# Optimization experiments

Hardware: AMD Instinct MI355X
Metric: run time of the kernel (lower is better)

The kernel has to match this reference:

```python
import jax, jax.numpy as jnp
import numpy as np

B, N, H, L, K = 8, 2048, 256, 4, 16
G, M0, M1, C = 512, 256, 128, 128
EPS = 1e-5


def _rn(k, shape, scale):
    return jax.random.normal(k, shape, jnp.float32) * jnp.float32(scale)


def setup_inputs() -> dict:
    key = jax.random.key(0)
    ks = jax.random.split(key, 16)
    z, o = jnp.zeros, jnp.ones
    return {
        "x": jax.random.normal(ks[0], (B, N, 3), jnp.float32),
        "batch": jnp.repeat(jnp.arange(B, dtype=jnp.int32)[:, None], N, axis=1),
        "Wf": _rn(ks[1], (3, H), 0.5), "bf": z(H),
        "Wnn": _rn(ks[2], (H, H), H ** -0.5), "bnn": z(H),
        "g1": o((L, H)), "b1": z((L, H)),
        "We": _rn(ks[3], (L, 2 * H, H), (2 * H) ** -0.5), "be": z((L, H)),
        "g2": o((L, H)), "b2": z((L, H)),
        "Wl": _rn(ks[4], (L, H, H), H ** -0.5), "bl": z((L, H)),
        "alpha": _rn(ks[5], (L,), 0.1),
        "gg": o(H), "bgb": z(H),
        "Wg": _rn(ks[6], (H, G), H ** -0.5), "bg2": z(G),
        "Wm1": _rn(ks[7], (G, M0), G ** -0.5), "bm1": z(M0),
        "Wm2": _rn(ks[8], (M0, M1), M0 ** -0.5), "bm2": z(M1),
        "Wm3": _rn(ks[9], (M1, C), M1 ** -0.5), "bm3": z(C),
    }


def _bn(x, g, b):
    # BatchNorm1d training-mode math over all nodes (axes B,N), per channel
    m = x.mean(axis=(0, 1))
    v = x.var(axis=(0, 1))
    return (x - m) * jax.lax.rsqrt(v + EPS) * g + b


def _dgcnn(x, We, be):
    # dynamic kNN graph in feature space, per cloud; x: [B,N,H]
    sq = jnp.sum(x * x, axis=-1)                                  # [B,N]
    d = sq[:, :, None] + sq[:, None, :] - 2.0 * jnp.einsum('bnd,bmd->bnm', x, x)
    idx = jax.lax.top_k(-d, K)[1]                                 # [B,N,K] (includes self)
    x_j = jax.vmap(lambda xb, ib: xb[ib])(x, idx)                 # [B,N,K,H]
    x_i = x[:, :, None, :]
    e = jnp.concatenate([jnp.broadcast_to(x_i, x_j.shape), x_j - x_i], axis=-1)
    msg = jnp.einsum('bnkf,fh->bnkh', e, We) + be                 # edge MLP
    return jnp.max(msg, axis=2)                                   # max aggregate


def _forward(x, Wf, bf, Wnn, bnn, g1, b1, We, be, g2, b2, Wl, bl, alpha,
             gg, bgb, Wg, bg2, Wm1, bm1, Wm2, bm2, Wm3, bm3):
    h = x @ Wf + bf                                               # ffm_x (Linear, scale=None)
    for i in range(L):
        t = h @ Wnn + bnn if i == 0 else h                        # nn_x only on first layer
        t = jax.nn.relu(_bn(t, g1[i], b1[i]))
        t = _dgcnn(t, We[i], be[i])
        t = jax.nn.relu(_bn(t, g2[i], b2[i]))
        t = t @ Wl[i] + bl[i]
        h = h + alpha[i] * t                                      # ResidualCoefficient
    t = jax.nn.relu(_bn(h, gg, bgb)) @ Wg + bg2
    p = jnp.max(t, axis=1)                                        # global max pool -> [B,G]
    p = jax.nn.relu(p @ Wm1 + bm1)
    p = jax.nn.relu(p @ Wm2 + bm2)
    return p @ Wm3 + bm3                                          # [B, n_components]


def reference(x, batch, Wf, bf, Wnn, bnn, g1, b1, We, be, g2, b2, Wl, bl, alpha,
              gg, bgb, Wg, bg2, Wm1, bm1, Wm2, bm2, Wm3, bm3):
    # batch ids are implied by the dense [B,N] layout; kept for signature fidelity
    del batch
    return _forward(x, Wf, bf, Wnn, bnn, g1, b1, We, be, g2, b2, Wl, bl, alpha,
                    gg, bgb, Wg, bg2, Wm1, bm1, Wm2, bm2, Wm3, bm3)
```

## Files before the change

### kernel.cpp

```cpp
#include <hip/hip_runtime.h>
#include <cfloat>

#define B_  8
#define N_  2048
#define H_  256
#define L_  4
#define K_  16
#define G_  512
#define M0_ 256
#define M1_ 128
#define C_  128
#define BN_ 16384
#define KP_ 768

typedef unsigned short ushort_t;
typedef __attribute__((ext_vector_type(8))) short short8;
typedef __attribute__((ext_vector_type(4))) float f32x4;

#define OFF_H     ((size_t)0)
#define OFF_APACK ((size_t)16777216)
#define OFF_WPK   ((size_t)46137344)
#define OFF_BCA   ((size_t)52035584)
#define OFF_STA   ((size_t)52043776)
#define OFF_SQ    ((size_t)67108864)
#define OFF_IDX   ((size_t)67174400)
#define OFF_P0    ((size_t)68231168)
#define OFF_D     ((size_t)69206016)
#define OFF_T     (OFF_D + (size_t)0)
#define OFF_UV    (OFF_D + (size_t)50331648)
#define OFF_PMAX  (OFF_D + (size_t)84672512)
#define WS_NEEDED ((size_t)203423744)

#define WPK_WNN   0
#define WPK_WL    256
#define WPK_WG    1280
#define WPK_QCAT  1792

static __device__ __forceinline__ ushort_t f2bf(float f) {
    unsigned u = __float_as_uint(f);
    unsigned r = (u + 0x7fffu + ((u >> 16) & 1u)) >> 16;
    return (ushort_t)r;
}
static __device__ __forceinline__ float bf2f(ushort_t h) {
    return __uint_as_float(((unsigned)h) << 16);
}
static __device__ __forceinline__ void pack3(float v, ushort_t* A, size_t base, int f) {
    ushort_t hi = f2bf(v);
    ushort_t lo = f2bf(v - bf2f(hi));
    A[base + f] = hi; A[base + H_ + f] = lo; A[base + 2 * H_ + f] = hi;
}


__global__ void feat_pack(const float* __restrict__ x, const float* __restrict__ Wf,
                          const float* __restrict__ bfv, float* __restrict__ h,
                          ushort_t* __restrict__ Ap) {
    int pt = blockIdx.x;
    int f  = threadIdx.x;
    float x0 = x[pt * 3 + 0], x1 = x[pt * 3 + 1], x2 = x[pt * 3 + 2];
    float v = x0 * Wf[f] + x1 * Wf[H_ + f] + x2 * Wf[2 * H_ + f] + bfv[f];
    h[(size_t)pt * H_ + f] = v;
    pack3(v, Ap, (size_t)pt * KP_, f);
}

__global__ void pack_all(const float* __restrict__ Wnn, const float* __restrict__ Wl,
                         const float* __restrict__ Wg, const float* __restrict__ We,
                         const float* __restrict__ be, ushort_t* __restrict__ Qp,
                         float* __restrict__ bcat) {
    int row = blockIdx.x, k = threadIdx.x;
    float w;
    if (row < 1792) {
        const float* W; int Nd, n;
        if (row < 256)        { W = Wnn; Nd = 256; n = row; }
        else if (row < 1280)  { int l = (row - 256) >> 8;
                                W = Wl + (size_t)l * (H_ * H_); Nd = 256; n = (row - 256) & 255; }
        else                  { W = Wg; Nd = 512; n = row - 1280; }
        w = W[(size_t)k * Nd + n];
    } else {
        int rr = row - 1792; int l = rr >> 9; int n = rr & 511;
        const float* We_l = We + (size_t)l * 2 * H_ * H_;
        if (n < H_) w = We_l[(size_t)k * H_ + n] - We_l[(size_t)H_ * H_ + (size_t)k * H_ + n];
        else        w = We_l[(size_t)H_ * H_ + (size_t)k * H_ + (n - H_)];
        if (k == 0) bcat[l * 512 + n] = (n < H_) ? be[l * H_ + n] : 0.f;
    }
    ushort_t hi = f2bf(w), lo = f2bf(w - bf2f(hi));
    size_t base = (size_t)row * KP_;
    Qp[base + k] = hi; Qp[base + H_ + k] = hi; Qp[base + 2 * H_ + k] = lo;
}

__global__ __launch_bounds__(256) void mfma_gemm(
    const ushort_t* __restrict__ P, const ushort_t* __restrict__ Q,
    const float* __restrict__ aux, float* __restrict__ out,
    int Kd, int ldOut, int mode, const float* __restrict__ resid,
    const float* __restrict__ alphap, int aidx, double* __restrict__ stats,
    int nx) {
    __shared__ __align__(16) ushort_t As[128 * 32];
    __shared__ __align__(16) ushort_t Bs[128 * 32];
    __shared__ float cs1[4][64], cs2[4][64];
    int i0, j0;
    if (nx) {
        int blk = blockIdx.x;
        int z = blk & 7;
        int rest = blk >> 3;
        int xb = rest % nx;
        int ys = rest / nx;
        i0 = (z * 16 + ys) * 128;
        j0 = xb * 128;
    } else {
        i0 = blockIdx.y * 128; j0 = blockIdx.x * 128;
    }
    int tid = threadIdx.x;
    int lane = tid & 63, wave = tid >> 6;
    int wm = wave & 1, wn = wave >> 1;
    int m16 = lane & 15, kq = (lane >> 4) * 8;

    f32x4 acc[4][4];
    f32x4 zero = {0.f, 0.f, 0.f, 0.f};
#pragma unroll
    for (int i = 0; i < 4; ++i)
#pragma unroll
        for (int j = 0; j < 4; ++j) acc[i][j] = zero;

    int srow = tid >> 2;
    int skc  = (tid & 3) * 8;

    for (int k0 = 0; k0 < Kd; k0 += 32) {
#pragma unroll
        for (int s = 0; s < 2; ++s) {
            int row = srow + s * 64;
            const ushort_t* gpA = P + (size_t)(i0 + row) * Kd + k0 + skc;
            const ushort_t* gpB = Q + (size_t)(j0 + row) * Kd + k0 + skc;
            __builtin_amdgcn_global_load_lds(
                (const __attribute__((address_space(1))) void*)gpA,
                (__attribute__((address_space(3))) void*)(As + (size_t)(wave * 64 + s * 256) * 8),
                16, 0, 0);
            __builtin_amdgcn_global_load_lds(
                (const __attribute__((address_space(1))) void*)gpB,
                (__attribute__((address_space(3))) void*)(Bs + (size_t)(wave * 64 + s * 256) * 8),
                16, 0, 0);
        }
        __syncthreads();
        short8 af[4], bfr[4];
#pragma unroll
        for (int fi = 0; fi < 4; ++fi)
            af[fi] = *(const short8*)(As + (wm * 64 + fi * 16 + m16) * 32 + kq);
#pragma unroll
        for (int fj = 0; fj < 4; ++fj)
            bfr[fj] = *(const short8*)(Bs + (wn * 64 + fj * 16 + m16) * 32 + kq);
#pragma unroll
        for (int fi = 0; fi < 4; ++fi)
#pragma unroll
            for (int fj = 0; fj < 4; ++fj)
                acc[fi][fj] = __builtin_amdgcn_mfma_f32_16x16x32_bf16(
                    af[fi], bfr[fj], acc[fi][fj], 0, 0, 0);
        __syncthreads();
    }
    float alpha = (mode == 2) ? alphap[aidx] : 0.f;
    int rbase = i0 + wm * 64 + (lane >> 4) * 4;
    int cbase = j0 + wn * 64 + m16;
    float s1[4] = {0.f, 0.f, 0.f, 0.f}, s2[4] = {0.f, 0.f, 0.f, 0.f};
#pragma unroll
    for (int fi = 0; fi < 4; ++fi) {
#pragma unroll
        for (int fj = 0; fj < 4; ++fj) {
            int c = cbase + fj * 16;
            float a = aux[c];
#pragma unroll
            for (int r = 0; r < 4; ++r) {
                int gr = rbase + fi * 16 + r;
                size_t oidx = (size_t)gr * ldOut + c;
                float val;
                if (mode == 2) val = resid[oidx] + alpha * (acc[fi][fj][r] + a);
                else           val = acc[fi][fj][r] + a;
                out[oidx] = val;
                s1[fj] += val; s2[fj] += val * val;
            }
        }
    }
    if (stats) {
#pragma unroll
        for (int fj = 0; fj < 4; ++fj) {
            float a1 = s1[fj], a2 = s2[fj];
            a1 += __shfl_xor(a1, 16); a1 += __shfl_xor(a1, 32);
            a2 += __shfl_xor(a2, 16); a2 += __shfl_xor(a2, 32);
            if ((lane >> 4) == 0) {
                cs1[wave][fj * 16 + m16] = a1;
                cs2[wave][fj * 16 + m16] = a2;
            }
        }
        __syncthreads();
        if (tid < 128) {
            int wnl = tid >> 6, cl = tid & 63;
            float t1 = cs1[2 * wnl][cl] + cs1[2 * wnl + 1][cl];
            float t2 = cs2[2 * wnl][cl] + cs2[2 * wnl + 1][cl];
            int c = j0 + tid;
            atomicAdd(&stats[c], (double)t1);
            atomicAdd(&stats[H_ + c], (double)t2);
        }
    }
}

__global__ __launch_bounds__(256) void gram_sym(const ushort_t* __restrict__ Ap,
                                                const float* __restrict__ sqb,
                                                float* __restrict__ D) {
    __shared__ __align__(16) ushort_t As[128 * 32];
    __shared__ __align__(16) ushort_t Bs[128 * 32];
    __shared__ __align__(16) float stg[4][1280];
    int blk = blockIdx.x;
    int z = blk & 7;
    int p = blk >> 3;
    int bi = 0, rem = p;
    while (rem >= 16 - bi) { rem -= 16 - bi; ++bi; }
    int bj = bi + rem;
    const ushort_t* Pz = Ap + (size_t)z * N_ * KP_;
    const float* sqz = sqb + (size_t)z * N_;
    float* Dz = D + (size_t)z * N_ * N_;
    int i0 = bi * 128, j0 = bj * 128;

    int tid = threadIdx.x;
    int lane = tid & 63, wave = tid >> 6;
    int wm = wave & 1, wn = wave >> 1;
    int m16 = lane & 15, q4 = lane >> 4;
    int kq = q4 * 8;

    f32x4 acc[4][4];
    f32x4 zero = {0.f, 0.f, 0.f, 0.f};
#pragma unroll
    for (int i = 0; i < 4; ++i)
#pragma unroll
        for (int j = 0; j < 4; ++j) acc[i][j] = zero;

    int srow = tid >> 2;
    int skc  = (tid & 3) * 8;

    for (int k0 = 0; k0 < KP_; k0 += 32) {
        int kb = (k0 < 256) ? k0 : ((k0 < 512) ? k0 + 256 : k0 - 256);
#pragma unroll
        for (int s = 0; s < 2; ++s) {
            int row = srow + s * 64;
            const ushort_t* gpA = Pz + (size_t)(i0 + row) * KP_ + k0 + skc;
            const ushort_t* gpB = Pz + (size_t)(j0 + row) * KP_ + kb + skc;
            __builtin_amdgcn_global_load_lds(
                (const __attribute__((address_space(1))) void*)gpA,
                (__attribute__((address_space(3))) void*)(As + (size_t)(wave * 64 + s * 256) * 8),
                16, 0, 0);
            __builtin_amdgcn_global_load_lds(
                (const __attribute__((address_space(1))) void*)gpB,
                (__attribute__((address_space(3))) void*)(Bs + (size_t)(wave * 64 + s * 256) * 8),
                16, 0, 0);
        }
        __syncthreads();
        short8 af[4], bfr[4];
#pragma unroll
        for (int fi = 0; fi < 4; ++fi)
            af[fi] = *(const short8*)(As + (wm * 64 + fi * 16 + m16) * 32 + kq);
#pragma unroll
        for (int fj = 0; fj < 4; ++fj)
            bfr[fj] = *(const short8*)(Bs + (wn * 64 + fj * 16 + m16) * 32 + kq);
#pragma unroll
        for (int fi = 0; fi < 4; ++fi)
#pragma unroll
            for (int fj = 0; fj < 4; ++fj)
                acc[fi][fj] = __builtin_amdgcn_mfma_f32_16x16x32_bf16(
                    af[fi], bfr[fj], acc[fi][fj], 0, 0, 0);
        __syncthreads();
    }

    float* sg = stg[wave];
    float scl[4];
#pragma unroll
    for (int fj = 0; fj < 4; ++fj) scl[fj] = sqz[j0 + wn * 64 + fj * 16 + m16];
    float sr[4][4];
#pragma unroll
    for (int fi = 0; fi < 4; ++fi) {
        float4 s4 = *(const float4*)(sqz + i0 + wm * 64 + fi * 16 + q4 * 4);
        sr[fi][0] = s4.x; sr[fi][1] = s4.y; sr[fi][2] = s4.z; sr[fi][3] = s4.w;
    }

    int rr = lane >> 2, cc = lane & 3;
#pragma unroll
    for (int fi = 0; fi < 4; ++fi) {
#pragma unroll
        for (int fj = 0; fj < 4; ++fj)
#pragma unroll
            for (int r = 0; r < 4; ++r)
                sg[(q4 * 4 + r) * 68 + fj * 16 + m16] = scl[fj] - 2.f * acc[fi][fj][r];
        float* drow = Dz + (size_t)(i0 + wm * 64 + fi * 16 + rr) * N_ + j0 + wn * 64;
#pragma unroll
        for (int t = 0; t < 4; ++t) {
            int chunk = cc + 4 * t;
            f32x4 o = *(const f32x4*)(sg + rr * 68 + chunk * 4);
            __builtin_nontemporal_store(o, (f32x4*)(drow + chunk * 4));
        }
    }

    if (bi != bj) {
#pragma unroll
        for (int fi = 0; fi < 4; ++fi) {
#pragma unroll
            for (int fj = 0; fj < 4; ++fj)
#pragma unroll
                for (int r = 0; r < 4; ++r)
                    sg[(fj * 16 + m16) * 20 + q4 * 4 + r] =
                        sr[fi][r] - 2.f * acc[fi][fj][r];
            int chunk = lane & 3;
#pragma unroll
            for (int u = 0; u < 4; ++u) {
                int cr = (lane >> 2) + 16 * u;
                f32x4 o = *(const f32x4*)(sg + cr * 20 + chunk * 4);
                __builtin_nontemporal_store(o,
                    (f32x4*)(Dz + (size_t)(j0 + wn * 64 + cr) * N_ +
                             i0 + wm * 64 + fi * 16 + chunk * 4));
            }
        }
    }
}

__global__ __launch_bounds__(256) void topk16(const float* __restrict__ D,
                                              int* __restrict__ idxb) {
    __shared__ unsigned long long cand[4][256];
    __shared__ int cnt[4];
    int w = threadIdx.x >> 6, lane = threadIdx.x & 63;
    int row = blockIdx.x * 4 + w;
    const float* dp = D + (size_t)row * N_;
    unsigned sk[32];
#pragma unroll
    for (int t = 0; t < 8; ++t) {
        f32x4 v4 = __builtin_nontemporal_load((const f32x4*)(dp + t * 256 + lane * 4));
#pragma unroll
        for (int j = 0; j < 4; ++j) {
            unsigned u = __float_as_uint(v4[j]);
            sk[t * 4 + j] = (u & 0x80000000u) ? ~u : (u | 0x80000000u);
        }
    }
    if (lane == 0) cnt[w] = 0;
    unsigned vm = sk[0];
#pragma unroll
    for (int i = 1; i < 32; ++i) vm = min(vm, sk[i]);
#pragma unroll
    for (int k = 2; k <= 64; k <<= 1) {
#pragma unroll
        for (int j = k >> 1; j > 0; j >>= 1) {
            unsigned pv = __shfl_xor(vm, j);
            bool up = ((lane & k) == 0);
            bool lower = ((lane & j) == 0);
            unsigned mn = min(vm, pv), mx = max(vm, pv);
            vm = (lower == up) ? mn : mx;
        }
    }
    unsigned T = __shfl(vm, 15);
    __syncthreads();
#pragma unroll
    for (int i = 0; i < 32; ++i) {
        if (sk[i] <= T) {
            unsigned col = (unsigned)((i >> 2) * 256 + lane * 4 + (i & 3));
            int s = atomicAdd(&cnt[w], 1);
            if (s < 256) cand[w][s] = ((unsigned long long)sk[i] << 32) | col;
        }
    }
    __syncthreads();
    int cn = cnt[w];
    if (cn <= 64) {
        unsigned long long mykey = (lane < cn) ? cand[w][lane] : ~0ull;
        for (int it = 0; it < 16; ++it) {
            unsigned long long best = mykey;
#pragma unroll
            for (int off = 32; off; off >>= 1) {
                unsigned long long o = __shfl_xor(best, off);
                if (o < best) best = o;
            }
            if (mykey == best) mykey = ~0ull;
            if (lane == 0) idxb[row * 16 + it] = (int)(unsigned)(best & 0xffffffffu);
        }
    } else if (cn <= 256) {
        for (int it = 0; it < 16; ++it) {
            unsigned long long best = ~0ull;
            for (int i = lane; i < cn; i += 64) {
                unsigned long long c = cand[w][i];
                if (c < best) best = c;
            }
#pragma unroll
            for (int off = 32; off; off >>= 1) {
                unsigned long long o = __shfl_xor(best, off);
                if (o < best) best = o;
            }
            for (int i = lane; i < cn; i += 64)
                if (cand[w][i] == best) cand[w][i] = ~0ull;
            if (lane == 0) idxb[row * 16 + it] = (int)(unsigned)(best & 0xffffffffu);
        }
    } else {
        unsigned mask = 0;
        for (int it = 0; it < 16; ++it) {
            unsigned long long key = ~0ull;
#pragma unroll
            for (int i = 0; i < 32; ++i) {
                if (!((mask >> i) & 1u)) {
                    unsigned long long k2 = ((unsigned long long)sk[i] << 32) |
                        (unsigned)((i >> 2) * 256 + lane * 4 + (i & 3));
                    if (k2 < key) key = k2;
                }
            }
#pragma unroll
            for (int off = 32; off; off >>= 1) {
                unsigned long long o = __shfl_xor(key, off);
                if (o < key) key = o;
            }
            unsigned jc = (unsigned)(key & 0xffffffffu);
            int li = ((jc & 255) >> 2);
            int ii = ((jc >> 8) << 2) | (jc & 3);
            if (lane == li) mask |= 1u << ii;
            if (lane == 0) idxb[row * 16 + it] = (int)jc;
        }
    }
}

__global__ void gather_max(const float* __restrict__ uv, const int* __restrict__ idxb,
                           float* __restrict__ outp, double* __restrict__ stats) {
    int blk = blockIdx.x;
    int b = blk & 7;
    int strip = blk >> 3;
    int r0 = b * N_ + strip * 32;
    int f = threadIdx.x;
    float s1 = 0.f, s2 = 0.f;
    for (int rr = 0; rr < 32; ++rr) {
        int row = r0 + rr;
        const int* ip = idxb + row * 16;
        float m = -FLT_MAX;
#pragma unroll
        for (int k = 0; k < 16; ++k) {
            int j = ip[k];
            m = fmaxf(m, uv[((size_t)((b << 11) + j)) * 512 + 256 + f]);
        }
        float v = uv[(size_t)row * 512 + f] + m;
        outp[(size_t)row * H_ + f] = v;
        s1 += v; s2 += v * v;
    }
    atomicAdd(&stats[f], (double)s1);
    atomicAdd(&stats[H_ + f], (double)s2);
}

__global__ void bn_zero(double* s) { s[(size_t)blockIdx.x * 512 + threadIdx.x] = 0.0; }

__global__ void bn_apply_pack(const float* __restrict__ X, const double* __restrict__ sums,
                              const float* __restrict__ g, const float* __restrict__ b,
                              ushort_t* __restrict__ Ap, float* __restrict__ sq) {
    __shared__ float scsh[512];
    int tid = threadIdx.x;
    {
        double m  = sums[tid] / (double)BN_;
        double var = sums[H_ + tid] / (double)BN_ - m * m;
        double inv = 1.0 / sqrt(var + 1e-5);
        float sc = g[tid] * (float)inv;
        scsh[tid] = sc;
        scsh[H_ + tid] = b[tid] - (float)m * sc;
    }
    __syncthreads();
    int row = blockIdx.x * 8 + (tid >> 5);
    int f0  = (tid & 31) * 8;
    const float* xp = X + (size_t)row * H_ + f0;
    f32x4 x0 = *(const f32x4*)(xp);
    f32x4 x1 = *(const f32x4*)(xp + 4);
    f32x4 sc0 = *(const f32x4*)(scsh + f0);
    f32x4 sc1 = *(const f32x4*)(scsh + f0 + 4);
    f32x4 sh0 = *(const f32x4*)(scsh + H_ + f0);
    f32x4 sh1 = *(const f32x4*)(scsh + H_ + f0 + 4);
    float v[8];
#pragma unroll
    for (int i = 0; i < 4; ++i) {
        v[i]     = fmaxf(x0[i] * sc0[i] + sh0[i], 0.f);
        v[i + 4] = fmaxf(x1[i] * sc1[i] + sh1[i], 0.f);
    }
    short8 hi8, lo8;
#pragma unroll
    for (int i = 0; i < 8; ++i) {
        ushort_t hi = f2bf(v[i]);
        ushort_t lo = f2bf(v[i] - bf2f(hi));
        hi8[i] = (short)hi; lo8[i] = (short)lo;
    }
    ushort_t* ap = Ap + (size_t)row * KP_ + f0;
    *(short8*)(ap)            = hi8;
    *(short8*)(ap + H_)       = lo8;
    *(short8*)(ap + 2 * H_)   = hi8;
    if (sq) {
        float s = 0.f;
#pragma unroll
        for (int i = 0; i < 8; ++i) s += v[i] * v[i];
#pragma unroll
        for (int off = 16; off; off >>= 1) s += __shfl_down(s, off, 32);
        if ((tid & 31) == 0) sq[row] = s;
    }
}

__global__ void maxpool1(const float* __restrict__ y, float* __restrict__ pmax) {
    int b = blockIdx.x, gc = blockIdx.y, nc = blockIdx.z;
    int g = gc * 256 + threadIdx.x;
    const float* yb = y + ((size_t)b * N_ + (size_t)nc * 128) * G_;
    float m = -FLT_MAX;
    for (int n = 0; n < 128; ++n) m = fmaxf(m, yb[(size_t)n * G_ + g]);
    pmax[((size_t)(b * 16 + nc)) * G_ + g] = m;
}

__global__ void maxpool2(const float* __restrict__ pmax, float* __restrict__ p) {
    int b = blockIdx.x;
    int g = blockIdx.y * 256 + threadIdx.x;
    float m = -FLT_MAX;
    for (int c = 0; c < 16; ++c) m = fmaxf(m, pmax[((size_t)(b * 16 + c)) * G_ + g]);
    p[(size_t)b * G_ + g] = m;
}

__global__ __launch_bounds__(256) void head3(const float* __restrict__ p0,
    const float* __restrict__ Wm1, const float* __restrict__ bm1,
    const float* __restrict__ Wm2, const float* __restrict__ bm2,
    const float* __restrict__ Wm3, const float* __restrict__ bm3,
    float* __restrict__ out) {
    __shared__ float s0[512];
    __shared__ float s1[256];
    __shared__ float red[4][64];
    int b = blockIdx.x, tid = threadIdx.x;
    s0[tid] = p0[(size_t)b * 512 + tid];
    s0[256 + tid] = p0[(size_t)b * 512 + 256 + tid];
    int cl = tid & 63, ks = tid >> 6;
    __syncthreads();
    for (int cg = 0; cg < 4; ++cg) {
        int c = cg * 64 + cl;
        const float* Apt = s0 + ks * 128;
        const float* Wp  = Wm1 + (size_t)(ks * 128) * M0_ + c;
        float acc = 0.f;
        for (int k = 0; k < 128; k += 8)
#pragma unroll
            for (int u2 = 0; u2 < 8; ++u2)
                acc += Apt[k + u2] * Wp[(size_t)(k + u2) * M0_];
        red[ks][cl] = acc;
        __syncthreads();
        if (ks == 0) {
            float s = red[0][cl] + red[1][cl] + red[2][cl] + red[3][cl] + bm1[c];
            s1[c] = fmaxf(s, 0.f);
        }
        __syncthreads();
    }
    float s2v[2];
    for (int cg = 0; cg < 2; ++cg) {
        int c = cg * 64 + cl;
        const float* Apt = s1 + ks * 64;
        const float* Wp  = Wm2 + (size_t)(ks * 64) * M1_ + c;
        float acc = 0.f;
        for (int k = 0; k < 64; k += 8)
#pragma unroll
            for (int u2 = 0; u2 < 8; ++u2)
                acc += Apt[k + u2] * Wp[(size_t)(k + u2) * M1_];
        red[ks][cl] = acc;
        __syncthreads();
        s2v[cg] = 0.f;
        if (ks == 0) {
            float s = red[0][cl] + red[1][cl] + red[2][cl] + red[3][cl] + bm2[c];
            s2v[cg] = fmaxf(s, 0.f);
        }
        __syncthreads();
    }
    if (ks == 0) { s0[cl] = s2v[0]; s0[64 + cl] = s2v[1]; }
    __syncthreads();
    for (int cg = 0; cg < 2; ++cg) {
        int c = cg * 64 + cl;
        const float* Apt = s0 + ks * 32;
        const float* Wp  = Wm3 + (size_t)(ks * 32) * C_ + c;
        float acc = 0.f;
        for (int k = 0; k < 32; k += 8)
#pragma unroll
            for (int u2 = 0; u2 < 8; ++u2)
                acc += Apt[k + u2] * Wp[(size_t)(k + u2) * C_];
        red[ks][cl] = acc;
        __syncthreads();
        if (ks == 0)
            out[(size_t)b * C_ + c] =
                red[0][cl] + red[1][cl] + red[2][cl] + red[3][cl] + bm3[c];
        __syncthreads();
    }
}

extern "C" void kernel_launch(void* const* d_in, const int* in_sizes, int n_in,
                              void* d_out, int out_size, void* d_ws, size_t ws_size,
                              hipStream_t stream) {
    (void)in_sizes; (void)n_in; (void)out_size;
    if (ws_size < WS_NEEDED) return;

    const float* x    = (const float*)d_in[0];
    const float* Wf   = (const float*)d_in[2];
    const float* bfv  = (const float*)d_in[3];
    const float* Wnn  = (const float*)d_in[4];
    const float* bnn  = (const float*)d_in[5];
    const float* g1   = (const float*)d_in[6];
    const float* b1   = (const float*)d_in[7];
    const float* We   = (const float*)d_in[8];
    const float* be   = (const float*)d_in[9];
    const float* g2   = (const float*)d_in[10];
    const float* b2   = (const float*)d_in[11];
    const float* Wl   = (const float*)d_in[12];
    const float* bl   = (const float*)d_in[13];
    const float* alpha= (const float*)d_in[14];
    const float* gg   = (const float*)d_in[15];
    const float* bgb  = (const float*)d_in[16];
    const float* Wg   = (const float*)d_in[17];
    const float* bg2  = (const float*)d_in[18];
    const float* Wm1  = (const float*)d_in[19];
    const float* bm1  = (const float*)d_in[20];
    const float* Wm2  = (const float*)d_in[21];
    const float* bm2  = (const float*)d_in[22];
    const float* Wm3  = (const float*)d_in[23];
    const float* bm3  = (const float*)d_in[24];
    float* outp = (float*)d_out;

    char* ws = (char*)d_ws;
    float*    h    = (float*)(ws + OFF_H);
    ushort_t* Ap   = (ushort_t*)(ws + OFF_APACK);
    ushort_t* Qpk  = (ushort_t*)(ws + OFF_WPK);
    float*    bcatA= (float*)(ws + OFF_BCA);
    double*   sta  = (double*)(ws + OFF_STA);
    float*    sqb  = (float*)(ws + OFF_SQ);
    int*      idxb = (int*)  (ws + OFF_IDX);
    float*    p0   = (float*)(ws + OFF_P0);
    float*    dmat = (float*)(ws + OFF_D);
    float*    t    = (float*)(ws + OFF_T);
    float*    uv   = (float*)(ws + OFF_UV);
    float*    y    = (float*)(ws + OFF_UV);
    float*    pmax = (float*)(ws + OFF_PMAX);

    ushort_t* Qwnn = Qpk + (size_t)WPK_WNN * KP_;
    ushort_t* Qwg  = Qpk + (size_t)WPK_WG  * KP_;

    hipLaunchKernelGGL(bn_zero, dim3(9), dim3(512), 0, stream, sta);
    hipLaunchKernelGGL(pack_all, dim3(3840), dim3(256), 0, stream,
                       Wnn, Wl, Wg, We, be, Qpk, bcatA);

    hipLaunchKernelGGL(feat_pack, dim3(BN_), dim3(256), 0, stream, x, Wf, bfv, h, Ap);
    hipLaunchKernelGGL(mfma_gemm, dim3(256), dim3(256), 0, stream,
                       Ap, Qwnn, bnn, t, KP_, H_, 0,
                       (const float*)nullptr, (const float*)nullptr, 0, sta, 2);

    for (int l = 0; l < L_; ++l) {
        const float* src1 = (l == 0) ? t : h;
        hipLaunchKernelGGL(bn_apply_pack, dim3(BN_ / 8), dim3(256), 0, stream,
                           src1, sta + (size_t)(2 * l) * 512,
                           g1 + l * H_, b1 + l * H_, Ap, sqb);
        hipLaunchKernelGGL(gram_sym, dim3(1088), dim3(256), 0, stream,
                           Ap, sqb, dmat);
        hipLaunchKernelGGL(topk16, dim3(BN_ / 4), dim3(256), 0, stream, dmat, idxb);
        hipLaunchKernelGGL(mfma_gemm, dim3(512), dim3(256), 0, stream,
                           Ap, Qpk + (size_t)(WPK_QCAT + l * 512) * KP_,
                           bcatA + (size_t)l * 512, uv, KP_, 512, 0,
                           (const float*)nullptr, (const float*)nullptr, 0,
                           (double*)nullptr, 4);
        hipLaunchKernelGGL(gather_max, dim3(512), dim3(256), 0, stream,
                           uv, idxb, t, sta + (size_t)(2 * l + 1) * 512);
        hipLaunchKernelGGL(bn_apply_pack, dim3(BN_ / 8), dim3(256), 0, stream,
                           t, sta + (size_t)(2 * l + 1) * 512,
                           g2 + l * H_, b2 + l * H_, Ap, (float*)nullptr);
        hipLaunchKernelGGL(mfma_gemm, dim3(256), dim3(256), 0, stream,
                           Ap, Qpk + (size_t)(WPK_WL + l * 256) * KP_,
                           bl + (size_t)l * H_, h, KP_, H_, 2,
                           h, alpha, l, sta + (size_t)(2 * l + 2) * 512, 2);
    }

    hipLaunchKernelGGL(bn_apply_pack, dim3(BN_ / 8), dim3(256), 0, stream,
                       h, sta + (size_t)8 * 512, gg, bgb, Ap, (float*)nullptr);
    hipLaunchKernelGGL(mfma_gemm, dim3(512), dim3(256), 0, stream,
                       Ap, Qwg, bg2, y, KP_, G_, 0,
                       (const float*)nullptr, (const float*)nullptr, 0,
                       (double*)nullptr, 4);
    hipLaunchKernelGGL(maxpool1, dim3(8, 2, 16), dim3(256), 0, stream, y, pmax);
    hipLaunchKernelGGL(maxpool2, dim3(8, 2), dim3(256), 0, stream, pmax, p0);
    hipLaunchKernelGGL(head3, dim3(8), dim3(256), 0, stream,
                       p0, Wm1, bm1, Wm2, bm2, Wm3, bm3, outp);
}
```

Baseline: 1.100 ms.

## Compact split-bf16 packing, fuse gram with edge GEMM, fuse head GEMM with maxpool

Packed activations and weights are stored as [hi, lo] (512 wide) instead of [hi, lo, hi] (768 wide). The three-term product is rebuilt by remapping K offsets in the loaders, which cuts pack writes and operand footprint. The prep, weight-pack and stat-zeroing kernels merge into one launch. When the workspace is large enough, the gram and edge-MLP GEMMs run in one combined launch. The final projection GEMM now does the max pooling in its epilogue, so the large intermediate is never written. These changes add workspace-size-dependent branching, and the fused path may not run if the workspace is smaller.

```diff
diff --git a/kernel.cpp b/kernel.cpp
--- a/kernel.cpp
+++ b/kernel.cpp
@@ -12,6 +12,7 @@
 #define C_  128
 #define BN_ 16384
 #define KP_ 768
+#define KPC_ 512
 
 typedef unsigned short ushort_t;
 typedef __attribute__((ext_vector_type(8))) short short8;
@@ -19,17 +20,16 @@
 
 #define OFF_H     ((size_t)0)
 #define OFF_APACK ((size_t)16777216)
-#define OFF_WPK   ((size_t)46137344)
-#define OFF_BCA   ((size_t)52035584)
-#define OFF_STA   ((size_t)52043776)
-#define OFF_SQ    ((size_t)67108864)
-#define OFF_IDX   ((size_t)67174400)
-#define OFF_P0    ((size_t)68231168)
-#define OFF_D     ((size_t)69206016)
-#define OFF_T     (OFF_D + (size_t)0)
-#define OFF_UV    (OFF_D + (size_t)50331648)
-#define OFF_PMAX  (OFF_D + (size_t)84672512)
-#define WS_NEEDED ((size_t)203423744)
+#define OFF_WPK   ((size_t)33554432)
+#define OFF_BCA   ((size_t)37486592)
+#define OFF_STA   ((size_t)37494784)
+#define OFF_SQ    ((size_t)37531648)
+#define OFF_IDX   ((size_t)37597184)
+#define OFF_UVBIG ((size_t)38645760)
+#define OFF_DSML  ((size_t)69206016)
+#define OFF_DBIG  ((size_t)72200192)
+#define WS_SMALL  ((size_t)203423744)
+#define WS_BIG    ((size_t)206417920)
 
 #define WPK_WNN   0
 #define WPK_WL    256
@@ -44,53 +44,57 @@
 static __device__ __forceinline__ float bf2f(ushort_t h) {
     return __uint_as_float(((unsigned)h) << 16);
 }
-static __device__ __forceinline__ void pack3(float v, ushort_t* A, size_t base, int f) {
-    ushort_t hi = f2bf(v);
-    ushort_t lo = f2bf(v - bf2f(hi));
-    A[base + f] = hi; A[base + H_ + f] = lo; A[base + 2 * H_ + f] = hi;
-}
-
-
-__global__ void feat_pack(const float* __restrict__ x, const float* __restrict__ Wf,
-                          const float* __restrict__ bfv, float* __restrict__ h,
-                          ushort_t* __restrict__ Ap) {
-    int pt = blockIdx.x;
-    int f  = threadIdx.x;
-    float x0 = x[pt * 3 + 0], x1 = x[pt * 3 + 1], x2 = x[pt * 3 + 2];
-    float v = x0 * Wf[f] + x1 * Wf[H_ + f] + x2 * Wf[2 * H_ + f] + bfv[f];
-    h[(size_t)pt * H_ + f] = v;
-    pack3(v, Ap, (size_t)pt * KP_, f);
-}
-
-__global__ void pack_all(const float* __restrict__ Wnn, const float* __restrict__ Wl,
-                         const float* __restrict__ Wg, const float* __restrict__ We,
-                         const float* __restrict__ be, ushort_t* __restrict__ Qp,
-                         float* __restrict__ bcat) {
-    int row = blockIdx.x, k = threadIdx.x;
-    float w;
-    if (row < 1792) {
-        const float* W; int Nd, n;
-        if (row < 256)        { W = Wnn; Nd = 256; n = row; }
-        else if (row < 1280)  { int l = (row - 256) >> 8;
-                                W = Wl + (size_t)l * (H_ * H_); Nd = 256; n = (row - 256) & 255; }
-        else                  { W = Wg; Nd = 512; n = row - 1280; }
-        w = W[(size_t)k * Nd + n];
+static __device__ __forceinline__ int kmapA(int k0) { return (k0 < KPC_) ? k0 : k0 - KPC_; }
+static __device__ __forceinline__ int kmapB(int k0) { return (k0 < 256)  ? k0 : k0 - 256; }
+
+__global__ void prep(const float* __restrict__ x, const float* __restrict__ Wf,
+                     const float* __restrict__ bfv, float* __restrict__ h,
+                     ushort_t* __restrict__ Ap,
+                     const float* __restrict__ Wnn, const float* __restrict__ Wl,
+                     const float* __restrict__ Wg, const float* __restrict__ We,
+                     const float* __restrict__ be, ushort_t* __restrict__ Qp,
+                     float* __restrict__ bcat, double* __restrict__ sta) {
+    int blk = blockIdx.x;
+    int tid = threadIdx.x;
+    if (blk < BN_) {
+        int pt = blk, f = tid;
+        float x0 = x[pt * 3 + 0], x1 = x[pt * 3 + 1], x2 = x[pt * 3 + 2];
+        float v = x0 * Wf[f] + x1 * Wf[H_ + f] + x2 * Wf[2 * H_ + f] + bfv[f];
+        h[(size_t)pt * H_ + f] = v;
+        ushort_t hi = f2bf(v), lo = f2bf(v - bf2f(hi));
+        size_t base = (size_t)pt * KPC_;
+        Ap[base + f] = hi; Ap[base + H_ + f] = lo;
+    } else if (blk < BN_ + 3840) {
+        int row = blk - BN_, k = tid;
+        float w;
+        if (row < 1792) {
+            const float* W; int Nd, n;
+            if (row < 256)        { W = Wnn; Nd = 256; n = row; }
+            else if (row < 1280)  { int l = (row - 256) >> 8;
+                                    W = Wl + (size_t)l * (H_ * H_); Nd = 256; n = (row - 256) & 255; }
+            else                  { W = Wg; Nd = 512; n = row - 1280; }
+            w = W[(size_t)k * Nd + n];
+        } else {
+            int rr = row - 1792; int l = rr >> 9; int n = rr & 511;
+            const float* We_l = We + (size_t)l * 2 * H_ * H_;
+            if (n < H_) w = We_l[(size_t)k * H_ + n] - We_l[(size_t)H_ * H_ + (size_t)k * H_ + n];
+            else        w = We_l[(size_t)H_ * H_ + (size_t)k * H_ + (n - H_)];
+            if (k == 0) bcat[l * 512 + n] = (n < H_) ? be[l * H_ + n] : 0.f;
+        }
+        ushort_t hi = f2bf(w), lo = f2bf(w - bf2f(hi));
+        size_t base = (size_t)row * KPC_;
+        Qp[base + k] = hi; Qp[base + H_ + k] = lo;
     } else {
-        int rr = row - 1792; int l = rr >> 9; int n = rr & 511;
-        const float* We_l = We + (size_t)l * 2 * H_ * H_;
-        if (n < H_) w = We_l[(size_t)k * H_ + n] - We_l[(size_t)H_ * H_ + (size_t)k * H_ + n];
-        else        w = We_l[(size_t)H_ * H_ + (size_t)k * H_ + (n - H_)];
-        if (k == 0) bcat[l * 512 + n] = (n < H_) ? be[l * H_ + n] : 0.f;
-    }
-    ushort_t hi = f2bf(w), lo = f2bf(w - bf2f(hi));
-    size_t base = (size_t)row * KP_;
-    Qp[base + k] = hi; Qp[base + H_ + k] = hi; Qp[base + 2 * H_ + k] = lo;
+        int slot = blk - (BN_ + 3840);
+        sta[(size_t)slot * 512 + tid] = 0.0;
+        sta[(size_t)slot * 512 + 256 + tid] = 0.0;
+    }
 }
 
 __global__ __launch_bounds__(256) void mfma_gemm(
     const ushort_t* __restrict__ P, const ushort_t* __restrict__ Q,
     const float* __restrict__ aux, float* __restrict__ out,
-    int Kd, int ldOut, int mode, const float* __restrict__ resid,
+    int ldOut, int mode, const float* __restrict__ resid,
     const float* __restrict__ alphap, int aidx, double* __restrict__ stats,
     int nx) {
     __shared__ __align__(16) ushort_t As[128 * 32];
@@ -123,12 +127,13 @@
     int srow = tid >> 2;
     int skc  = (tid & 3) * 8;
 
-    for (int k0 = 0; k0 < Kd; k0 += 32) {
+    for (int k0 = 0; k0 < KP_; k0 += 32) {
+        int ka = kmapA(k0), kb = kmapB(k0);
 #pragma unroll
         for (int s = 0; s < 2; ++s) {
             int row = srow + s * 64;
-            const ushort_t* gpA = P + (size_t)(i0 + row) * Kd + k0 + skc;
-            const ushort_t* gpB = Q + (size_t)(j0 + row) * Kd + k0 + skc;
+            const ushort_t* gpA = P + (size_t)(i0 + row) * KPC_ + ka + skc;
+            const ushort_t* gpB = Q + (size_t)(j0 + row) * KPC_ + kb + skc;
             __builtin_amdgcn_global_load_lds(
                 (const __attribute__((address_space(1))) void*)gpA,
                 (__attribute__((address_space(3))) void*)(As + (size_t)(wave * 64 + s * 256) * 8),
@@ -199,6 +204,192 @@
     }
 }
 
+static __device__ __forceinline__ void gram_body(
+    ushort_t* As, ushort_t* Bs, float* sg,
+    const ushort_t* __restrict__ Pz, const float* __restrict__ sqz,
+    float* __restrict__ Dz, int bi, int bj) {
+    int i0 = bi * 128, j0 = bj * 128;
+    int tid = threadIdx.x;
+    int lane = tid & 63, wave = tid >> 6;
+    int wm = wave & 1, wn = wave >> 1;
+    int m16 = lane & 15, q4 = lane >> 4;
+    int kq = q4 * 8;
+
+    f32x4 acc[4][4];
+    f32x4 zero = {0.f, 0.f, 0.f, 0.f};
+#pragma unroll
+    for (int i = 0; i < 4; ++i)
+#pragma unroll
+        for (int j = 0; j < 4; ++j) acc[i][j] = zero;
+
+    int srow = tid >> 2;
+    int skc  = (tid & 3) * 8;
+
+    for (int k0 = 0; k0 < KP_; k0 += 32) {
+        int ka = kmapA(k0), kb = kmapB(k0);
+#pragma unroll
+        for (int s = 0; s < 2; ++s) {
+            int row = srow + s * 64;
+            const ushort_t* gpA = Pz + (size_t)(i0 + row) * KPC_ + ka + skc;
+            const ushort_t* gpB = Pz + (size_t)(j0 + row) * KPC_ + kb + skc;
+            __builtin_amdgcn_global_load_lds(
+                (const __attribute__((address_space(1))) void*)gpA,
+                (__attribute__((address_space(3))) void*)(As + (size_t)(wave * 64 + s * 256) * 8),
+                16, 0, 0);
+            __builtin_amdgcn_global_load_lds(
+                (const __attribute__((address_space(1))) void*)gpB,
+                (__attribute__((address_space(3))) void*)(Bs + (size_t)(wave * 64 + s * 256) * 8),
+                16, 0, 0);
+        }
+        __syncthreads();
+        short8 af[4], bfr[4];
+#pragma unroll
+        for (int fi = 0; fi < 4; ++fi)
+            af[fi] = *(const short8*)(As + (wm * 64 + fi * 16 + m16) * 32 + kq);
+#pragma unroll
+        for (int fj = 0; fj < 4; ++fj)
+            bfr[fj] = *(const short8*)(Bs + (wn * 64 + fj * 16 + m16) * 32 + kq);
+#pragma unroll
+        for (int fi = 0; fi < 4; ++fi)
+#pragma unroll
+            for (int fj = 0; fj < 4; ++fj)
+                acc[fi][fj] = __builtin_amdgcn_mfma_f32_16x16x32_bf16(
+                    af[fi], bfr[fj], acc[fi][fj], 0, 0, 0);
+        __syncthreads();
+    }
+
+    float scl[4];
+#pragma unroll
+    for (int fj = 0; fj < 4; ++fj) scl[fj] = sqz[j0 + wn * 64 + fj * 16 + m16];
+    float sr[4][4];
+#pragma unroll
+    for (int fi = 0; fi < 4; ++fi) {
+        float4 s4 = *(const float4*)(sqz + i0 + wm * 64 + fi * 16 + q4 * 4);
+        sr[fi][0] = s4.x; sr[fi][1] = s4.y; sr[fi][2] = s4.z; sr[fi][3] = s4.w;
+    }
+
+    int rr = lane >> 2, cc = lane & 3;
+#pragma unroll
+    for (int fi = 0; fi < 4; ++fi) {
+#pragma unroll
+        for (int fj = 0; fj < 4; ++fj)
+#pragma unroll
+            for (int r = 0; r < 4; ++r)
+                sg[(q4 * 4 + r) * 68 + fj * 16 + m16] = scl[fj] - 2.f * acc[fi][fj][r];
+        float* drow = Dz + (size_t)(i0 + wm * 64 + fi * 16 + rr) * N_ + j0 + wn * 64;
+#pragma unroll
+        for (int t = 0; t < 4; ++t) {
+            int chunk = cc + 4 * t;
+            f32x4 o = *(const f32x4*)(sg + rr * 68 + chunk * 4);
+            __builtin_nontemporal_store(o, (f32x4*)(drow + chunk * 4));
+        }
+    }
+
+    if (bi != bj) {
+#pragma unroll
+        for (int fi = 0; fi < 4; ++fi) {
+#pragma unroll
+            for (int fj = 0; fj < 4; ++fj)
+#pragma unroll
+                for (int r = 0; r < 4; ++r)
+                    sg[(fj * 16 + m16) * 20 + q4 * 4 + r] =
+                        sr[fi][r] - 2.f * acc[fi][fj][r];
+            int chunk = lane & 3;
+#pragma unroll
+            for (int u = 0; u < 4; ++u) {
+                int cr = (lane >> 2) + 16 * u;
+                f32x4 o = *(const f32x4*)(sg + cr * 20 + chunk * 4);
+                __builtin_nontemporal_store(o,
+                    (f32x4*)(Dz + (size_t)(j0 + wn * 64 + cr) * N_ +
+                             i0 + wm * 64 + fi * 16 + chunk * 4));
+            }
+        }
+    }
+}
+
+static __device__ __forceinline__ void pair_decode(int p, int* pbi, int* pbj) {
+    if (p < 120) {
+        int bi = 0, rem = p;
+        while (rem >= 15 - bi) { rem -= 15 - bi; ++bi; }
+        *pbi = bi; *pbj = bi + 1 + rem;
+    } else {
+        *pbi = *pbj = p - 120;
+    }
+}
+
+static __device__ __forceinline__ void uvgemm_body(
+    ushort_t* As, ushort_t* Bs,
+    const ushort_t* __restrict__ P, const ushort_t* __restrict__ Q,
+    const float* __restrict__ aux, float* __restrict__ out, int ublk) {
+    int z = ublk & 7;
+    int rest = ublk >> 3;
+    int xb = rest & 3;
+    int ys = rest >> 2;
+    int i0 = (z * 16 + ys) * 128;
+    int j0 = xb * 128;
+    int tid = threadIdx.x;
+    int lane = tid & 63, wave = tid >> 6;
+    int wm = wave & 1, wn = wave >> 1;
+    int m16 = lane & 15, kq = (lane >> 4) * 8;
+
+    f32x4 acc[4][4];
+    f32x4 zero = {0.f, 0.f, 0.f, 0.f};
+#pragma unroll
+    for (int i = 0; i < 4; ++i)
+#pragma unroll
+        for (int j = 0; j < 4; ++j) acc[i][j] = zero;
+
+    int srow = tid >> 2;
+    int skc  = (tid & 3) * 8;
+
+    for (int k0 = 0; k0 < KP_; k0 += 32) {
+        int ka = kmapA(k0), kb = kmapB(k0);
+#pragma unroll
+        for (int s = 0; s < 2; ++s) {
+            int row = srow + s * 64;
+            const ushort_t* gpA = P + (size_t)(i0 + row) * KPC_ + ka + skc;
+            const ushort_t* gpB = Q + (size_t)(j0 + row) * KPC_ + kb + skc;
+            __builtin_amdgcn_global_load_lds(
+                (const __attribute__((address_space(1))) void*)gpA,
+                (__attribute__((address_space(3))) void*)(As + (size_t)(wave * 64 + s * 256) * 8),
+                16, 0, 0);
+            __builtin_amdgcn_global_load_lds(
+                (const __attribute__((address_space(1))) void*)gpB,
+                (__attribute__((address_space(3))) void*)(Bs + (size_t)(wave * 64 + s * 256) * 8),
+                16, 0, 0);
+        }
+        __syncthreads();
+        short8 af[4], bfr[4];
+#pragma unroll
+        for (int fi = 0; fi < 4; ++fi)
+            af[fi] = *(const short8*)(As + (wm * 64 + fi * 16 + m16) * 32 + kq);
+#pragma unroll
+        for (int fj = 0; fj < 4; ++fj)
+            bfr[fj] = *(const short8*)(Bs + (wn * 64 + fj * 16 + m16) * 32 + kq);
+#pragma unroll
+        for (int fi = 0; fi < 4; ++fi)
+#pragma unroll
+            for (int fj = 0; fj < 4; ++fj)
+                acc[fi][fj] = __builtin_amdgcn_mfma_f32_16x16x32_bf16(
+                    af[fi], bfr[fj], acc[fi][fj], 0, 0, 0);
+        __syncthreads();
+    }
+    int rbase = i0 + wm * 64 + (lane >> 4) * 4;
+    int cbase = j0 + wn * 64 + m16;
+#pragma unroll
+    for (int fi = 0; fi < 4; ++fi)
+#pragma unroll
+        for (int fj = 0; fj < 4; ++fj) {
+            int c = cbase + fj * 16;
+            float a = aux[c];
+#pragma unroll
+            for (int r = 0; r < 4; ++r) {
+                int gr = rbase + fi * 16 + r;
+                out[(size_t)gr * 512 + c] = acc[fi][fj][r] + a;
+            }
+        }
+}
+
 __global__ __launch_bounds__(256) void gram_sym(const ushort_t* __restrict__ Ap,
                                                 const float* __restrict__ sqb,
                                                 float* __restrict__ D) {
@@ -207,112 +398,35 @@
     __shared__ __align__(16) float stg[4][1280];
     int blk = blockIdx.x;
     int z = blk & 7;
-    int p = blk >> 3;
-    int bi = 0, rem = p;
-    while (rem >= 16 - bi) { rem -= 16 - bi; ++bi; }
-    int bj = bi + rem;
-    const ushort_t* Pz = Ap + (size_t)z * N_ * KP_;
-    const float* sqz = sqb + (size_t)z * N_;
-    float* Dz = D + (size_t)z * N_ * N_;
-    int i0 = bi * 128, j0 = bj * 128;
-
-    int tid = threadIdx.x;
-    int lane = tid & 63, wave = tid >> 6;
-    int wm = wave & 1, wn = wave >> 1;
-    int m16 = lane & 15, q4 = lane >> 4;
-    int kq = q4 * 8;
-
-    f32x4 acc[4][4];
-    f32x4 zero = {0.f, 0.f, 0.f, 0.f};
-#pragma unroll
-    for (int i = 0; i < 4; ++i)
-#pragma unroll
-        for (int j = 0; j < 4; ++j) acc[i][j] = zero;
-
-    int srow = tid >> 2;
-    int skc  = (tid & 3) * 8;
-
-    for (int k0 = 0; k0 < KP_; k0 += 32) {
-        int kb = (k0 < 256) ? k0 : ((k0 < 512) ? k0 + 256 : k0 - 256);
-#pragma unroll
-        for (int s = 0; s < 2; ++s) {
-            int row = srow + s * 64;
-            const ushort_t* gpA = Pz + (size_t)(i0 + row) * KP_ + k0 + skc;
-            const ushort_t* gpB = Pz + (size_t)(j0 + row) * KP_ + kb + skc;
-            __builtin_amdgcn_global_load_lds(
-                (const __attribute__((address_space(1))) void*)gpA,
-                (__attribute__((address_space(3))) void*)(As + (size_t)(wave * 64 + s * 256) * 8),
-                16, 0, 0);
-            __builtin_amdgcn_global_load_lds(
-                (const __attribute__((address_space(1))) void*)gpB,
-                (__attribute__((address_space(3))) void*)(Bs + (size_t)(wave * 64 + s * 256) * 8),
-                16, 0, 0);
-        }
-        __syncthreads();
-        short8 af[4], bfr[4];
-#pragma unroll
-        for (int fi = 0; fi < 4; ++fi)
-            af[fi] = *(const short8*)(As + (wm * 64 + fi * 16 + m16) * 32 + kq);
-#pragma unroll
-        for (int fj = 0; fj < 4; ++fj)
-            bfr[fj] = *(const short8*)(Bs + (wn * 64 + fj * 16 + m16) * 32 + kq);
-#pragma unroll
-        for (int fi = 0; fi < 4; ++fi)
-#pragma unroll
-            for (int fj = 0; fj < 4; ++fj)
-                acc[fi][fj] = __builtin_amdgcn_mfma_f32_16x16x32_bf16(
-                    af[fi], bfr[fj], acc[fi][fj], 0, 0, 0);
-        __syncthreads();
-    }
-
-    float* sg = stg[wave];
-    float scl[4];
-#pragma unroll
-    for (int fj = 0; fj < 4; ++fj) scl[fj] = sqz[j0 + wn * 64 + fj * 16 + m16];
-    float sr[4][4];
-#pragma unroll
-    for (int fi = 0; fi < 4; ++fi) {
-        float4 s4 = *(const float4*)(sqz + i0 + wm * 64 + fi * 16 + q4 * 4);
-        sr[fi][0] = s4.x; sr[fi][1] = s4.y; sr[fi][2] = s4.z; sr[fi][3] = s4.w;
-    }
-
-    int rr = lane >> 2, cc = lane & 3;
-#pragma unroll
-    for (int fi = 0; fi < 4; ++fi) {
-#pragma unroll
-        for (int fj = 0; fj < 4; ++fj)
-#pragma unroll
-            for (int r = 0; r < 4; ++r)
-                sg[(q4 * 4 + r) * 68 + fj * 16 + m16] = scl[fj] - 2.f * acc[fi][fj][r];
-        float* drow = Dz + (size_t)(i0 + wm * 64 + fi * 16 + rr) * N_ + j0 + wn * 64;
-#pragma unroll
-        for (int t = 0; t < 4; ++t) {
-            int chunk = cc + 4 * t;
-            f32x4 o = *(const f32x4*)(sg + rr * 68 + chunk * 4);
-            __builtin_nontemporal_store(o, (f32x4*)(drow + chunk * 4));
-        }
-    }
-
-    if (bi != bj) {
-#pragma unroll
-        for (int fi = 0; fi < 4; ++fi) {
-#pragma unroll
-            for (int fj = 0; fj < 4; ++fj)
-#pragma unroll
-                for (int r = 0; r < 4; ++r)
-                    sg[(fj * 16 + m16) * 20 + q4 * 4 + r] =
-                        sr[fi][r] - 2.f * acc[fi][fj][r];
-            int chunk = lane & 3;
-#pragma unroll
-            for (int u = 0; u < 4; ++u) {
-                int cr = (lane >> 2) + 16 * u;
-                f32x4 o = *(const f32x4*)(sg + cr * 20 + chunk * 4);
-                __builtin_nontemporal_store(o,
-                    (f32x4*)(Dz + (size_t)(j0 + wn * 64 + cr) * N_ +
-                             i0 + wm * 64 + fi * 16 + chunk * 4));
-            }
-        }
-    }
+    int p = (blk < 960) ? (blk >> 3) : (120 + ((blk - 960) >> 3));
+    int bi, bj;
+    pair_decode(p, &bi, &bj);
+    gram_body(As, Bs, stg[threadIdx.x >> 6],
+              Ap + (size_t)z * N_ * KPC_, sqb + (size_t)z * N_,
+              D + (size_t)z * N_ * N_, bi, bj);
+}
+
+__global__ __launch_bounds__(256) void gram_uv(const ushort_t* __restrict__ Ap,
+                                               const float* __restrict__ sqb,
+                                               float* __restrict__ D,
+                                               const ushort_t* __restrict__ Qcat,
+                                               const float* __restrict__ bcat,
+                                               float* __restrict__ uv) {
+    __shared__ __align__(16) ushort_t As[128 * 32];
+    __shared__ __align__(16) ushort_t Bs[128 * 32];
+    __shared__ __align__(16) float stg[4][1280];
+    int blk = blockIdx.x;
+    if (blk >= 960 && blk < 1472) {
+        uvgemm_body(As, Bs, Ap, Qcat, bcat, uv, blk - 960);
+        return;
+    }
+    int z = blk & 7;
+    int p = (blk < 960) ? (blk >> 3) : (120 + ((blk - 1472) >> 3));
+    int bi, bj;
+    pair_decode(p, &bi, &bj);
+    gram_body(As, Bs, stg[threadIdx.x >> 6],
+              Ap + (size_t)z * N_ * KPC_, sqb + (size_t)z * N_,
+              D + (size_t)z * N_ * N_, bi, bj);
 }
 
 __global__ __launch_bounds__(256) void topk16(const float* __restrict__ D,
@@ -438,8 +552,6 @@
     atomicAdd(&stats[H_ + f], (double)s2);
 }
 
-__global__ void bn_zero(double* s) { s[(size_t)blockIdx.x * 512 + threadIdx.x] = 0.0; }
-
 __global__ void bn_apply_pack(const float* __restrict__ X, const double* __restrict__ sums,
                               const float* __restrict__ g, const float* __restrict__ b,
                               ushort_t* __restrict__ Ap, float* __restrict__ sq) {
@@ -476,10 +588,9 @@
         ushort_t lo = f2bf(v[i] - bf2f(hi));
         hi8[i] = (short)hi; lo8[i] = (short)lo;
     }
-    ushort_t* ap = Ap + (size_t)row * KP_ + f0;
-    *(short8*)(ap)            = hi8;
-    *(short8*)(ap + H_)       = lo8;
-    *(short8*)(ap + 2 * H_)   = hi8;
+    ushort_t* ap = Ap + (size_t)row * KPC_ + f0;
+    *(short8*)(ap)      = hi8;
+    *(short8*)(ap + H_) = lo8;
     if (sq) {
         float s = 0.f;
 #pragma unroll
@@ -490,24 +601,95 @@
     }
 }
 
-__global__ void maxpool1(const float* __restrict__ y, float* __restrict__ pmax) {
-    int b = blockIdx.x, gc = blockIdx.y, nc = blockIdx.z;
-    int g = gc * 256 + threadIdx.x;
-    const float* yb = y + ((size_t)b * N_ + (size_t)nc * 128) * G_;
-    float m = -FLT_MAX;
-    for (int n = 0; n < 128; ++n) m = fmaxf(m, yb[(size_t)n * G_ + g]);
-    pmax[((size_t)(b * 16 + nc)) * G_ + g] = m;
-}
-
-__global__ void maxpool2(const float* __restrict__ pmax, float* __restrict__ p) {
-    int b = blockIdx.x;
-    int g = blockIdx.y * 256 + threadIdx.x;
-    float m = -FLT_MAX;
-    for (int c = 0; c < 16; ++c) m = fmaxf(m, pmax[((size_t)(b * 16 + c)) * G_ + g]);
-    p[(size_t)b * G_ + g] = m;
-}
-
-__global__ __launch_bounds__(256) void head3(const float* __restrict__ p0,
+__global__ __launch_bounds__(256) void head_gemm_pool(
+    const ushort_t* __restrict__ P, const ushort_t* __restrict__ Q,
+    const float* __restrict__ aux, float* __restrict__ pmax) {
+    __shared__ __align__(16) ushort_t As[128 * 32];
+    __shared__ __align__(16) ushort_t Bs[128 * 32];
+    __shared__ float smax[2][2][64];
+    int blk = blockIdx.x;
+    int z = blk & 7;
+    int rest = blk >> 3;
+    int xb = rest & 3;
+    int ys = rest >> 2;
+    int i0 = (z * 16 + ys) * 128;
+    int j0 = xb * 128;
+    int tid = threadIdx.x;
+    int lane = tid & 63, wave = tid >> 6;
+    int wm = wave & 1, wn = wave >> 1;
+    int m16 = lane & 15, kq = (lane >> 4) * 8;
+
+    f32x4 acc[4][4];
+    f32x4 zero = {0.f, 0.f, 0.f, 0.f};
+#pragma unroll
+    for (int i = 0; i < 4; ++i)
+#pragma unroll
+        for (int j = 0; j < 4; ++j) acc[i][j] = zero;
+
+    int srow = tid >> 2;
+    int skc  = (tid & 3) * 8;
+
+    for (int k0 = 0; k0 < KP_; k0 += 32) {
+        int ka = kmapA(k0), kb = kmapB(k0);
+#pragma unroll
+        for (int s = 0; s < 2; ++s) {
+            int row = srow + s * 64;
+            const ushort_t* gpA = P + (size_t)(i0 + row) * KPC_ + ka + skc;
+            const ushort_t* gpB = Q + (size_t)(j0 + row) * KPC_ + kb + skc;
+            __builtin_amdgcn_global_load_lds(
+                (const __attribute__((address_space(1))) void*)gpA,
+                (__attribute__((address_space(3))) void*)(As + (size_t)(wave * 64 + s * 256) * 8),
+                16, 0, 0);
+            __builtin_amdgcn_global_load_lds(
+                (const __attribute__((address_space(1))) void*)gpB,
+                (__attribute__((address_space(3))) void*)(Bs + (size_t)(wave * 64 + s * 256) * 8),
+                16, 0, 0);
+        }
+        __syncthreads();
+        short8 af[4], bfr[4];
+#pragma unroll
+        for (int fi = 0; fi < 4; ++fi)
+            af[fi] = *(const short8*)(As + (wm * 64 + fi * 16 + m16) * 32 + kq);
+#pragma unroll
+        for (int fj = 0; fj < 4; ++fj)
+            bfr[fj] = *(const short8*)(Bs + (wn * 64 + fj * 16 + m16) * 32 + kq);
+#pragma unroll
+        for (int fi = 0; fi < 4; ++fi)
+#pragma unroll
+            for (int fj = 0; fj < 4; ++fj)
+                acc[fi][fj] = __builtin_amdgcn_mfma_f32_16x16x32_bf16(
+                    af[fi], bfr[fj], acc[fi][fj], 0, 0, 0);
+        __syncthreads();
+    }
+    float vmax[4];
+#pragma unroll
+    for (int fj = 0; fj < 4; ++fj) {
+        int c = j0 + wn * 64 + m16 + fj * 16;
+        float a = aux[c];
+        float m = -FLT_MAX;
+#pragma unroll
+        for (int fi = 0; fi < 4; ++fi)
+#pragma unroll
+            for (int r = 0; r < 4; ++r)
+                m = fmaxf(m, acc[fi][fj][r] + a);
+        m = fmaxf(m, __shfl_xor(m, 16));
+        m = fmaxf(m, __shfl_xor(m, 32));
+        vmax[fj] = m;
+    }
+    if (lane < 16) {
+#pragma unroll
+        for (int fj = 0; fj < 4; ++fj)
+            smax[wm][wn][fj * 16 + m16] = vmax[fj];
+    }
+    __syncthreads();
+    if (tid < 128) {
+        int wn2 = tid >> 6, off = tid & 63;
+        float m = fmaxf(smax[0][wn2][off], smax[1][wn2][off]);
+        pmax[((size_t)(z * 16 + ys)) * G_ + j0 + wn2 * 64 + off] = m;
+    }
+}
+
+__global__ __launch_bounds__(256) void head3(const float* __restrict__ pmax,
     const float* __restrict__ Wm1, const float* __restrict__ bm1,
     const float* __restrict__ Wm2, const float* __restrict__ bm2,
     const float* __restrict__ Wm3, const float* __restrict__ bm3,
@@ -516,8 +698,14 @@
     __shared__ float s1[256];
     __shared__ float red[4][64];
     int b = blockIdx.x, tid = threadIdx.x;
-    s0[tid] = p0[(size_t)b * 512 + tid];
-    s0[256 + tid] = p0[(size_t)b * 512 + 256 + tid];
+    {
+        float m0 = -FLT_MAX, m1 = -FLT_MAX;
+        for (int c2 = 0; c2 < 16; ++c2) {
+            m0 = fmaxf(m0, pmax[((size_t)(b * 16 + c2)) * G_ + tid]);
+            m1 = fmaxf(m1, pmax[((size_t)(b * 16 + c2)) * G_ + 256 + tid]);
+        }
+        s0[tid] = m0; s0[256 + tid] = m1;
+    }
     int cl = tid & 63, ks = tid >> 6;
     __syncthreads();
     for (int cg = 0; cg < 4; ++cg) {
@@ -580,7 +768,8 @@
                               void* d_out, int out_size, void* d_ws, size_t ws_size,
                               hipStream_t stream) {
     (void)in_sizes; (void)n_in; (void)out_size;
-    if (ws_size < WS_NEEDED) return;
+    if (ws_size < WS_SMALL) return;
+    const bool big = (ws_size >= WS_BIG);
 
     const float* x    = (const float*)d_in[0];
     const float* Wf   = (const float*)d_in[2];
@@ -616,23 +805,22 @@
     double*   sta  = (double*)(ws + OFF_STA);
     float*    sqb  = (float*)(ws + OFF_SQ);
     int*      idxb = (int*)  (ws + OFF_IDX);
-    float*    p0   = (float*)(ws + OFF_P0);
-    float*    dmat = (float*)(ws + OFF_D);
-    float*    t    = (float*)(ws + OFF_T);
-    float*    uv   = (float*)(ws + OFF_UV);
-    float*    y    = (float*)(ws + OFF_UV);
-    float*    pmax = (float*)(ws + OFF_PMAX);
-
-    ushort_t* Qwnn = Qpk + (size_t)WPK_WNN * KP_;
-    ushort_t* Qwg  = Qpk + (size_t)WPK_WG  * KP_;
-
-    hipLaunchKernelGGL(bn_zero, dim3(9), dim3(512), 0, stream, sta);
-    hipLaunchKernelGGL(pack_all, dim3(3840), dim3(256), 0, stream,
-                       Wnn, Wl, Wg, We, be, Qpk, bcatA);
-
-    hipLaunchKernelGGL(feat_pack, dim3(BN_), dim3(256), 0, stream, x, Wf, bfv, h, Ap);
+
+    size_t offD = big ? OFF_DBIG : OFF_DSML;
+    float*    dmat = (float*)(ws + offD);
+    float*    t    = (float*)(ws + offD);
+    float*    uv   = big ? (float*)(ws + OFF_UVBIG)
+                         : (float*)(ws + offD + (size_t)50331648);
+    float*    pmax = (float*)(ws + offD + (size_t)84672512);
+
+    ushort_t* Qwnn = Qpk + (size_t)WPK_WNN * KPC_;
+    ushort_t* Qwg  = Qpk + (size_t)WPK_WG  * KPC_;
+
+    hipLaunchKernelGGL(prep, dim3(BN_ + 3840 + 9), dim3(256), 0, stream,
+                       x, Wf, bfv, h, Ap, Wnn, Wl, Wg, We, be, Qpk, bcatA, sta);
+
     hipLaunchKernelGGL(mfma_gemm, dim3(256), dim3(256), 0, stream,
-                       Ap, Qwnn, bnn, t, KP_, H_, 0,
+                       Ap, Qwnn, bnn, t, H_, 0,
                        (const float*)nullptr, (const float*)nullptr, 0, sta, 2);
 
     for (int l = 0; l < L_; ++l) {
@@ -640,33 +828,37 @@
         hipLaunchKernelGGL(bn_apply_pack, dim3(BN_ / 8), dim3(256), 0, stream,
                            src1, sta + (size_t)(2 * l) * 512,
                            g1 + l * H_, b1 + l * H_, Ap, sqb);
-        hipLaunchKernelGGL(gram_sym, dim3(1088), dim3(256), 0, stream,
-                           Ap, sqb, dmat);
-        hipLaunchKernelGGL(topk16, dim3(BN_ / 4), dim3(256), 0, stream, dmat, idxb);
-        hipLaunchKernelGGL(mfma_gemm, dim3(512), dim3(256), 0, stream,
-                           Ap, Qpk + (size_t)(WPK_QCAT + l * 512) * KP_,
-                           bcatA + (size_t)l * 512, uv, KP_, 512, 0,
-                           (const float*)nullptr, (const float*)nullptr, 0,
-                           (double*)nullptr, 4);
+        if (big) {
+            hipLaunchKernelGGL(gram_uv, dim3(1600), dim3(256), 0, stream,
+                               Ap, sqb, dmat,
+                               Qpk + (size_t)(WPK_QCAT + l * 512) * KPC_,
+                               bcatA + (size_t)l * 512, uv);
+            hipLaunchKernelGGL(topk16, dim3(BN_ / 4), dim3(256), 0, stream, dmat, idxb);
+        } else {
+            hipLaunchKernelGGL(gram_sym, dim3(1088), dim3(256), 0, stream,
+                               Ap, sqb, dmat);
+            hipLaunchKernelGGL(topk16, dim3(BN_ / 4), dim3(256), 0, stream, dmat, idxb);
+            hipLaunchKernelGGL(mfma_gemm, dim3(512), dim3(256), 0, stream,
+                               Ap, Qpk + (size_t)(WPK_QCAT + l * 512) * KPC_,
+                               bcatA + (size_t)l * 512, uv, 512, 0,
+                               (const float*)nullptr, (const float*)nullptr, 0,
+                               (double*)nullptr, 4);
+        }
         hipLaunchKernelGGL(gather_max, dim3(512), dim3(256), 0, stream,
                            uv, idxb, t, sta + (size_t)(2 * l + 1) * 512);
         hipLaunchKernelGGL(bn_apply_pack, dim3(BN_ / 8), dim3(256), 0, stream,
                            t, sta + (size_t)(2 * l + 1) * 512,
                            g2 + l * H_, b2 + l * H_, Ap, (float*)nullptr);
         hipLaunchKernelGGL(mfma_gemm, dim3(256), dim3(256), 0, stream,
-                           Ap, Qpk + (size_t)(WPK_WL + l * 256) * KP_,
-                           bl + (size_t)l * H_, h, KP_, H_, 2,
+                           Ap, Qpk + (size_t)(WPK_WL + l * 256) * KPC_,
+                           bl + (size_t)l * H_, h, H_, 2,
                            h, alpha, l, sta + (size_t)(2 * l + 2) * 512, 2);
     }
 
     hipLaunchKernelGGL(bn_apply_pack, dim3(BN_ / 8), dim3(256), 0, stream,
                        h, sta + (size_t)8 * 512, gg, bgb, Ap, (float*)nullptr);
-    hipLaunchKernelGGL(mfma_gemm, dim3(512), dim3(256), 0, stream,
-                       Ap, Qwg, bg2, y, KP_, G_, 0,
-                       (const float*)nullptr, (const float*)nullptr, 0,
-                       (double*)nullptr, 4);
-    hipLaunchKernelGGL(maxpool1, dim3(8, 2, 16), dim3(256), 0, stream, y, pmax);
-    hipLaunchKernelGGL(maxpool2, dim3(8, 2), dim3(256), 0, stream, pmax, p0);
+    hipLaunchKernelGGL(head_gemm_pool, dim3(512), dim3(256), 0, stream,
+                       Ap, Qwg, bg2, pmax);
     hipLaunchKernelGGL(head3, dim3(8), dim3(256), 0, stream,
-                       p0, Wm1, bm1, Wm2, bm2, Wm3, bm3, outp);
-}
+                       pmax, Wm1, bm1, Wm2, bm2, Wm3, bm3, outp);
+}
```

Measured after the change: 1.048 ms. 4.7% less time.
